# Performance work log

Measured on AMD Instinct MI355X. Metric: run time of the kernel, lower is better.

Reference implementation:

```python
import math
import jax, jax.numpy as jnp
import numpy as np

N_HEADS = 16
HIDDEN = 1024
FACTOR = 256
N_DK = HIDDEN // N_HEADS
B, S = 4, 2048


def _linear_params(key, fan_in, fan_out):
    kw, kb = jax.random.split(key)
    bound = 1.0 / math.sqrt(fan_in)
    W = jax.random.uniform(kw, (fan_in, fan_out), jnp.float32, -bound, bound)
    b = jax.random.uniform(kb, (fan_out,), jnp.float32, -bound, bound)
    return W, b


def setup_inputs() -> dict:
    key = jax.random.key(0)
    ks = jax.random.split(key, 12)
    inp = {
        "query": jax.random.normal(ks[0], (B, S, HIDDEN), jnp.float32),
        "key": jax.random.normal(ks[1], (B, S, HIDDEN), jnp.float32),
        "value": jax.random.normal(ks[2], (B, S, HIDDEN), jnp.float32),
        "mask": jax.random.randint(ks[3], (B, S), 0, 2, jnp.int32),
    }
    names = [("pq", HIDDEN, FACTOR), ("tq", FACTOR, HIDDEN),
             ("pk", HIDDEN, FACTOR), ("tk", FACTOR, HIDDEN),
             ("pv", HIDDEN, FACTOR), ("tv", FACTOR, HIDDEN),
             ("po", HIDDEN, FACTOR), ("to", FACTOR, HIDDEN)]
    for i, (nm, fi, fo) in enumerate(names):
        W, b = _linear_params(ks[4 + i], fi, fo)
        inp[f"W{nm}"], inp[f"b{nm}"] = W, b
    return inp


def _factored(x, Wp, bp, Wt, bt):
    # proj -> leaky_relu(0.2) -> tran
    h = jax.nn.leaky_relu(x @ Wp + bp, negative_slope=0.2)
    return h @ Wt + bt


def reference(query, key, value, mask,
              Wpq, bpq, Wtq, btq, Wpk, bpk, Wtk, btk,
              Wpv, bpv, Wtv, btv, Wpo, bpo, Wto, bto):
    bsize = query.shape[0]

    def split_heads(x):  # [B,S,H*Dk] -> [B,H,S,Dk]
        return x.reshape(bsize, -1, N_HEADS, N_DK).transpose(0, 2, 1, 3)

    q = split_heads(_factored(query, Wpq, bpq, Wtq, btq))
    k = split_heads(_factored(key, Wpk, bpk, Wtk, btk))
    v = split_heads(_factored(value, Wpv, bpv, Wtv, btv))

    scores = jnp.einsum("bhqd,bhkd->bhqk", q, k) / math.sqrt(N_DK)
    m = (mask == 0)[:, None, None, :]  # [B,1,1,S]
    scores = jnp.where(m, jnp.float32(-1e20), scores)
    attn = jax.nn.softmax(scores, axis=-1)
    cv = jnp.einsum("bhqk,bhkd->bhqd", attn, v)
    cv = cv.transpose(0, 2, 1, 3).reshape(bsize, -1, N_HEADS * N_DK)
    # dropout omitted (eval mode / deterministic reference)
    return _factored(cv, Wpo, bpo, Wto, bto)
```

## Files before the change

### kernel.cpp

```cpp
#include <hip/hip_runtime.h>
#include <cstdint>
#include <cstddef>

typedef __bf16 bf16_t;
typedef __bf16 bf16x8 __attribute__((ext_vector_type(8)));
typedef float  f32x4  __attribute__((ext_vector_type(4)));
typedef unsigned int uint32x4 __attribute__((ext_vector_type(4)));
typedef unsigned int uint32x2 __attribute__((ext_vector_type(2)));

#define DEV_INLINE __device__ __forceinline__

constexpr int Bsz = 4, Ssz = 2048, HID = 1024, FAC = 256, NH = 16, DKc = 64;
constexpr int Mrows = Bsz * Ssz;
constexpr float QSCALE = 0.18033688011112042f;

struct Ptr8 { const float* p[8]; };
struct Ptr3 { const float* p[3]; };

DEV_INLINE float fast_exp2(float x) {
#if __has_builtin(__builtin_amdgcn_exp2f)
  return __builtin_amdgcn_exp2f(x);
#else
  return exp2f(x);
#endif
}

DEV_INLINE void async16(const void* g, void* l) {
  __builtin_amdgcn_global_load_lds((const __attribute__((address_space(1))) void*)g,
                                   (__attribute__((address_space(3))) void*)l, 16, 0, 0);
}

DEV_INLINE int SW(int r) { return (r & 3) | ((r >> 1) & 4); }

__global__ __launch_bounds__(256) void k_prep(Ptr8 w, Ptr8 bsrc, const int* __restrict__ mask,
                                              bf16_t* wpt, bf16_t* wtt,
                                              float* bp, float* bt, float* mf, bf16_t* mb) {
  const int z = blockIdx.z;
  if (z == 8) {
    const int bid = blockIdx.y * 32 + blockIdx.x;
    if (bid >= 64) return;
    const int i = bid * 256 + threadIdx.x;
    if (i < 4 * FAC) bp[i] = bsrc.p[i >> 8][i & 255];
    if (i < 4 * HID) bt[i] = bsrc.p[4 + (i >> 10)][i & 1023];
    if (i < Bsz * Ssz) {
      const float m = (mask[i] != 0) ? 1.f : 0.f;
      mf[i] = m;
      mb[i] = (bf16_t)m;
    }
    return;
  }
  const int K = (z < 4) ? HID : FAC;
  const int N = (z < 4) ? FAC : HID;
  if ((int)(blockIdx.x * 32) >= N || (int)(blockIdx.y * 32) >= K) return;
  __shared__ float t[32][33];
  const float* src = w.p[z];
  bf16_t* dst = (z < 4) ? (wpt + (size_t)z * FAC * HID) : (wtt + (size_t)(z - 4) * FAC * HID);
  const int tx = threadIdx.x & 31, ty = threadIdx.x >> 5;
  const int kb = blockIdx.y * 32, nb = blockIdx.x * 32;
#pragma unroll
  for (int j = 0; j < 4; ++j)
    t[ty + j * 8][tx] = src[(size_t)(kb + ty + j * 8) * N + nb + tx];
  __syncthreads();
#pragma unroll
  for (int j = 0; j < 4; ++j)
    dst[(size_t)(nb + ty + j * 8) * K + kb + tx] = (bf16_t)t[tx][ty + j * 8];
}

template <int CAST_A, typename OUT_T>
__global__ __launch_bounds__(256) void k_gemmP(Ptr3 Asrc,
                                               const bf16_t* __restrict__ Aall,
                                               const bf16_t* __restrict__ Bt_,
                                               const float* __restrict__ biasAll,
                                               OUT_T* __restrict__ Call,
                                               int K,
                                               long long Az, long long Bz, long long Cz, int biasz) {
  constexpr int LDTA = CAST_A ? 40 : 32;
  __shared__ __align__(16) bf16_t As[2][64 * LDTA];
  __shared__ __align__(16) bf16_t Bs[2][128 * 32];

  const int z = blockIdx.z;
  const bf16_t* Bt = Bt_ + (size_t)z * Bz;
  const float* bias = biasAll + (size_t)z * biasz;
  OUT_T* C = Call + (size_t)z * Cz;

  const int tid = threadIdx.x;
  const int lane = tid & 63, wave = tid >> 6;
  const int quad = lane >> 4, l16 = lane & 15;
  const int m0 = blockIdx.y * 64, n0 = blockIdx.x * 128;

  const int arow = wave * 16 + (lane >> 2), akc = (lane & 3) * 8;
  const bf16_t* gB0 = Bt + (size_t)(n0 + arow) * K + akc;
  const bf16_t* gB1 = gB0 + (size_t)64 * K;

  const float* gAf = nullptr;
  const bf16_t* gA = nullptr;
  const int crow = tid >> 2, chalf = (tid & 3) * 8;
  if (CAST_A) gAf = Asrc.p[z] + (size_t)(m0 + crow) * K + chalf;
  else        gA  = Aall + (size_t)z * Az + (size_t)(m0 + arow) * K + akc;

  async16(gB0, Bs[0] + wave * 512);
  async16(gB1, Bs[0] + 2048 + wave * 512);
  if (CAST_A) {
    f32x4 x0 = *(const f32x4*)gAf;
    f32x4 x1 = *(const f32x4*)(gAf + 4);
    union { bf16_t h[8]; uint32x4 u; } o;
#pragma unroll
    for (int j = 0; j < 4; ++j) { o.h[j] = (bf16_t)x0[j]; o.h[4 + j] = (bf16_t)x1[j]; }
    *(uint32x4*)(As[0] + crow * LDTA + chalf) = o.u;
  } else {
    async16(gA, As[0] + wave * 512);
  }

  f32x4 acc[4][2] = {};
  const int nk = K / 32;

  for (int it = 0; it < nk; ++it) {
    const int cur = it & 1, nxt = cur ^ 1;
    __syncthreads();

    f32x4 xa, xb;
    const int k1 = (it + 1) * 32;
    if (it + 1 < nk) {
      async16(gB0 + k1, Bs[nxt] + wave * 512);
      async16(gB1 + k1, Bs[nxt] + 2048 + wave * 512);
      if (CAST_A) {
        xa = *(const f32x4*)(gAf + k1);
        xb = *(const f32x4*)(gAf + k1 + 4);
      } else {
        async16(gA + k1, As[nxt] + wave * 512);
      }
    }

    bf16x8 af[4], bfr[2];
#pragma unroll
    for (int i = 0; i < 4; ++i)
      af[i] = *(const bf16x8*)(As[cur] + (i * 16 + l16) * LDTA + quad * 8);
#pragma unroll
    for (int i = 0; i < 2; ++i)
      bfr[i] = *(const bf16x8*)(Bs[cur] + (wave * 32 + i * 16 + l16) * 32 + quad * 8);
#pragma unroll
    for (int mi = 0; mi < 4; ++mi)
#pragma unroll
      for (int ni = 0; ni < 2; ++ni)
        acc[mi][ni] = __builtin_amdgcn_mfma_f32_16x16x32_bf16(af[mi], bfr[ni], acc[mi][ni], 0, 0, 0);

    if (CAST_A && it + 1 < nk) {
      union { bf16_t h[8]; uint32x4 u; } o;
#pragma unroll
      for (int j = 0; j < 4; ++j) { o.h[j] = (bf16_t)xa[j]; o.h[4 + j] = (bf16_t)xb[j]; }
      *(uint32x4*)(As[nxt] + crow * LDTA + chalf) = o.u;
    }
  }

#pragma unroll
  for (int mi = 0; mi < 4; ++mi) {
    const int rbase = m0 + mi * 16 + quad * 4;
#pragma unroll
    for (int ni = 0; ni < 2; ++ni) {
      const int col = n0 + wave * 32 + ni * 16 + l16;
      const float bv = bias[col];
#pragma unroll
      for (int r = 0; r < 4; ++r) {
        float y = acc[mi][ni][r] + bv;
        y = (y > 0.f) ? y : 0.2f * y;
        C[(size_t)(rbase + r) * FAC + col] = (OUT_T)y;
      }
    }
  }
}

template <int TVW, typename OUT_T>
__global__ __launch_bounds__(256) void k_gemm(const bf16_t* __restrict__ Aall,
                                              const bf16_t* __restrict__ Btall,
                                              const float* __restrict__ biasAll,
                                              OUT_T* __restrict__ Call,
                                              bf16_t* __restrict__ C2,
                                              const float* __restrict__ rowmul,
                                              int N, int K,
                                              long long Az, long long Bz, long long Cz, int biasz,
                                              float sc0, float sc1) {
  __shared__ __align__(16) bf16_t As[2][128 * 32];
  __shared__ __align__(16) bf16_t Bs[2][128 * 32];

  const int z = blockIdx.z;
  const bf16_t* Bt = Btall + (size_t)z * Bz;
  const float* bias = biasAll + (size_t)z * biasz;
  OUT_T* C = Call + (size_t)z * Cz;
  const float scale = (z == 0) ? sc0 : sc1;

  const int tid = threadIdx.x;
  const int lane = tid & 63, wave = tid >> 6;
  const int quad = lane >> 4, l16 = lane & 15;
  const int wr = wave >> 1, wc = wave & 1;
  const int m0 = blockIdx.y * 128, n0 = blockIdx.x * 128;

  const int arow = wave * 16 + (lane >> 2), akc = (lane & 3) * 8;
  const bf16_t* gB0 = Bt + (size_t)(n0 + arow) * K + akc;
  const bf16_t* gB1 = gB0 + (size_t)64 * K;
  const bf16_t* A = Aall + (size_t)z * Az;
  const bf16_t* gA0 = A + (size_t)(m0 + arow) * K + akc;
  const bf16_t* gA1 = gA0 + (size_t)64 * K;

  async16(gB0, Bs[0] + wave * 512);
  async16(gB1, Bs[0] + 2048 + wave * 512);
  async16(gA0, As[0] + wave * 512);
  async16(gA1, As[0] + 2048 + wave * 512);

  f32x4 acc[4][4] = {};
  const int nk = K / 32;

  for (int it = 0; it < nk; ++it) {
    const int cur = it & 1, nxt = cur ^ 1;
    __syncthreads();

    if (it + 1 < nk) {
      const int k1 = (it + 1) * 32;
      async16(gB0 + k1, Bs[nxt] + wave * 512);
      async16(gB1 + k1, Bs[nxt] + 2048 + wave * 512);
      async16(gA0 + k1, As[nxt] + wave * 512);
      async16(gA1 + k1, As[nxt] + 2048 + wave * 512);
    }

    bf16x8 af[4], bfr[4];
#pragma unroll
    for (int i = 0; i < 4; ++i)
      af[i] = *(const bf16x8*)(As[cur] + (wr * 64 + i * 16 + l16) * 32 + quad * 8);
#pragma unroll
    for (int i = 0; i < 4; ++i)
      bfr[i] = *(const bf16x8*)(Bs[cur] + (wc * 64 + i * 16 + l16) * 32 + quad * 8);
#pragma unroll
    for (int mi = 0; mi < 4; ++mi)
#pragma unroll
      for (int ni = 0; ni < 4; ++ni)
        acc[mi][ni] = __builtin_amdgcn_mfma_f32_16x16x32_bf16(af[mi], bfr[ni], acc[mi][ni], 0, 0, 0);
  }

  if (TVW && z == 2) {
#pragma unroll
    for (int mi = 0; mi < 4; ++mi) {
      const int rbase = m0 + wr * 64 + mi * 16 + quad * 4;
      const int bb = rbase >> 11, s = rbase & 2047;
      float rmv[4];
#pragma unroll
      for (int r = 0; r < 4; ++r) rmv[r] = rowmul[rbase + r];
#pragma unroll
      for (int ni = 0; ni < 4; ++ni) {
        const int col = n0 + wc * 64 + ni * 16 + l16;
        const float bv = bias[col];
        const int h = col >> 6, d = col & 63;
        union { bf16_t e[4]; uint32x2 u; } p;
#pragma unroll
        for (int r = 0; r < 4; ++r) p.e[r] = (bf16_t)((acc[mi][ni][r] + bv) * rmv[r]);
        *(uint32x2*)(C2 + (((size_t)((bb * NH + h) * DKc + d)) << 11) + s) = p.u;
      }
    }
    return;
  }

#pragma unroll
  for (int mi = 0; mi < 4; ++mi) {
    const int rbase = m0 + wr * 64 + mi * 16 + quad * 4;
#pragma unroll
    for (int ni = 0; ni < 4; ++ni) {
      const int col = n0 + wc * 64 + ni * 16 + l16;
      const float bv = bias[col];
#pragma unroll
      for (int r = 0; r < 4; ++r) {
        float y = (acc[mi][ni][r] + bv) * scale;
        C[(size_t)(rbase + r) * N + col] = (OUT_T)y;
      }
    }
  }
}

__global__ __launch_bounds__(512, 4) void k_attn(const bf16_t* __restrict__ qkv,
                                                 const bf16_t* __restrict__ mb,
                                                 bf16_t* __restrict__ cv) {
  __shared__ __align__(16) bf16_t Ks[2][64 * 64];
  __shared__ __align__(16) bf16_t Vt[2][64 * 64];
  __shared__ __align__(16) bf16_t Ml[Ssz];

  const int qt = blockIdx.x, h = blockIdx.y, b = blockIdx.z;
  const bf16_t* qp = qkv;
  const bf16_t* kp = qkv + (size_t)Mrows * HID;
  const bf16_t* vtp = qkv + 2 * (size_t)Mrows * HID + (size_t)(b * NH + h) * DKc * Ssz;

  const int tid = threadIdx.x;
  const int lane = tid & 63, wave = tid >> 6;
  const int quad = lane >> 4, l16 = lane & 15;

  const int r0 = wave * 8 + (lane >> 3);
  const int c0 = ((lane & 7) ^ SW(r0)) * 8;
  const int ldsOff = wave * 512;
  const bf16_t* kgA = kp + (size_t)(b * Ssz + r0) * HID + h * DKc + c0;
  const bf16_t* vgA = vtp + (size_t)r0 * Ssz + c0;

  *(uint32x2*)(Ml + tid * 4) = *(const uint32x2*)(mb + (size_t)b * Ssz + tid * 4);
  async16(kgA, Ks[0] + ldsOff);
  async16(vgA, Vt[0] + ldsOff);

  bf16x8 aq0[2], aq1[2];
#pragma unroll
  for (int g = 0; g < 2; ++g) {
    const size_t qrow = (size_t)(b * Ssz + qt * 256 + g * 128 + wave * 16 + l16) * HID + h * DKc + quad * 8;
    aq0[g] = *(const bf16x8*)(qp + qrow);
    aq1[g] = *(const bf16x8*)(qp + qrow + 32);
  }
  __syncthreads();

  const int krow = 8 * (l16 >> 2) + (l16 & 3);
  f32x4 acc[2][4] = {};
  f32x4 dacc[2] = {};
  const bf16x8 zfrag = {};

  for (int kt = 0; kt < 32; ++kt) {
    const int cur = kt & 1, nxt = cur ^ 1;
    if (kt < 31) {
      const size_t ko = (size_t)(kt + 1) * 64 * HID;
      const int vo = (kt + 1) * 64;
      async16(kgA + ko, Ks[nxt] + ldsOff);
      async16(vgA + vo, Vt[nxt] + ldsOff);
    }

    union U { uint32x4 u; bf16x8 h; } ap0[2], ap1[2];
    constexpr int koff[4] = {0, 4, 32, 36};
#pragma unroll
    for (int ks = 0; ks < 4; ++ks) {
      const int row = krow + koff[ks];
      const int sw = SW(row);
      bf16x8 a0 = *(const bf16x8*)(Ks[cur] + row * 64 + (quad ^ sw) * 8);
      bf16x8 a1 = *(const bf16x8*)(Ks[cur] + row * 64 + ((quad + 4) ^ sw) * 8);
#pragma unroll
      for (int g = 0; g < 2; ++g) {
        f32x4 c = {};
        c = __builtin_amdgcn_mfma_f32_16x16x32_bf16(a0, aq0[g], c, 0, 0, 0);
        c = __builtin_amdgcn_mfma_f32_16x16x32_bf16(a1, aq1[g], c, 0, 0, 0);
        union { bf16_t h[2]; uint32_t u; } p01, p23;
        p01.h[0] = (bf16_t)fast_exp2(c[0]);
        p01.h[1] = (bf16_t)fast_exp2(c[1]);
        p23.h[0] = (bf16_t)fast_exp2(c[2]);
        p23.h[1] = (bf16_t)fast_exp2(c[3]);
        U& t = (ks < 2) ? ap0[g] : ap1[g];
        t.u[(ks & 1) * 2] = p01.u;
        t.u[(ks & 1) * 2 + 1] = p23.u;
      }
    }

    bf16x8 mr0 = *(const bf16x8*)(Ml + kt * 64 + quad * 8);
    bf16x8 mr1 = *(const bf16x8*)(Ml + kt * 64 + 32 + quad * 8);
    if (l16 != 0) { mr0 = zfrag; mr1 = zfrag; }
#pragma unroll
    for (int g = 0; g < 2; ++g) {
      dacc[g] = __builtin_amdgcn_mfma_f32_16x16x32_bf16(ap0[g].h, mr0, dacc[g], 0, 0, 0);
      dacc[g] = __builtin_amdgcn_mfma_f32_16x16x32_bf16(ap1[g].h, mr1, dacc[g], 0, 0, 0);
    }

#pragma unroll
    for (int d = 0; d < 4; ++d) {
      const int row = d * 16 + l16;
      const int sw = SW(row);
      bf16x8 bv0 = *(const bf16x8*)(Vt[cur] + row * 64 + (quad ^ sw) * 8);
      bf16x8 bv1 = *(const bf16x8*)(Vt[cur] + row * 64 + ((quad + 4) ^ sw) * 8);
#pragma unroll
      for (int g = 0; g < 2; ++g) {
        acc[g][d] = __builtin_amdgcn_mfma_f32_16x16x32_bf16(ap0[g].h, bv0, acc[g][d], 0, 0, 0);
        acc[g][d] = __builtin_amdgcn_mfma_f32_16x16x32_bf16(ap1[g].h, bv1, acc[g][d], 0, 0, 0);
      }
    }

    __syncthreads();
  }

#pragma unroll
  for (int g = 0; g < 2; ++g) {
    const size_t obase = (size_t)(b * Ssz + qt * 256 + g * 128 + wave * 16 + quad * 4) * HID + h * DKc + l16;
#pragma unroll
    for (int r = 0; r < 4; ++r) {
      const float denom = __shfl(dacc[g][r], lane & 48, 64);
      const float rl = 1.f / denom;
#pragma unroll
      for (int d = 0; d < 4; ++d)
        cv[obase + (size_t)r * HID + d * 16] = (bf16_t)(acc[g][d][r] * rl);
    }
  }
}

extern "C" void kernel_launch(void* const* d_in, const int* in_sizes, int n_in,
                              void* d_out, int out_size, void* d_ws, size_t ws_size,
                              hipStream_t stream) {
  (void)in_sizes; (void)n_in; (void)out_size; (void)ws_size;
  const float* q_in = (const float*)d_in[0];
  const float* k_in = (const float*)d_in[1];
  const float* v_in = (const float*)d_in[2];
  const int* mask = (const int*)d_in[3];

  bf16_t* XB = (bf16_t*)d_ws;
  bf16_t* H3 = XB + (size_t)3 * Mrows * HID;
  bf16_t* CV = H3 + (size_t)3 * Mrows * FAC;
  bf16_t* WPT = CV + (size_t)Mrows * HID;
  bf16_t* WTT = WPT + (size_t)4 * FAC * HID;
  float* BP = (float*)(WTT + (size_t)4 * FAC * HID);
  float* BT = BP + 4 * FAC;
  float* MF = BT + 4 * HID;
  bf16_t* MB = (bf16_t*)(MF + Mrows);
  bf16_t* VTg = XB + 2 * (size_t)Mrows * HID;

  Ptr8 w;
  w.p[0] = (const float*)d_in[4];  w.p[1] = (const float*)d_in[8];
  w.p[2] = (const float*)d_in[12]; w.p[3] = (const float*)d_in[16];
  w.p[4] = (const float*)d_in[6];  w.p[5] = (const float*)d_in[10];
  w.p[6] = (const float*)d_in[14]; w.p[7] = (const float*)d_in[18];
  Ptr8 bs;
  bs.p[0] = (const float*)d_in[5];  bs.p[1] = (const float*)d_in[9];
  bs.p[2] = (const float*)d_in[13]; bs.p[3] = (const float*)d_in[17];
  bs.p[4] = (const float*)d_in[7];  bs.p[5] = (const float*)d_in[11];
  bs.p[6] = (const float*)d_in[15]; bs.p[7] = (const float*)d_in[19];
  hipLaunchKernelGGL(k_prep, dim3(32, 32, 9), dim3(256), 0, stream, w, bs, mask,
                     WPT, WTT, BP, BT, MF, MB);

  Ptr3 xs; xs.p[0] = q_in; xs.p[1] = k_in; xs.p[2] = v_in;
  Ptr3 nullp; nullp.p[0] = nullp.p[1] = nullp.p[2] = nullptr;

  hipLaunchKernelGGL((k_gemmP<1, bf16_t>), dim3(2, Mrows / 64, 3), dim3(256), 0, stream,
                     xs, (const bf16_t*)nullptr, WPT, BP, H3,
                     HID, 0LL, (long long)FAC * HID, (long long)Mrows * FAC, FAC);

  hipLaunchKernelGGL((k_gemm<1, bf16_t>), dim3(HID / 128, Mrows / 128, 3), dim3(256), 0, stream,
                     H3, WTT, BT, XB, VTg, MF,
                     HID, FAC, (long long)Mrows * FAC, (long long)FAC * HID, (long long)Mrows * HID, HID,
                     QSCALE, 1.f);

  hipLaunchKernelGGL(k_attn, dim3(Ssz / 256, NH, Bsz), dim3(512), 0, stream, XB, MB, CV);

  hipLaunchKernelGGL((k_gemmP<0, bf16_t>), dim3(2, Mrows / 64, 1), dim3(256), 0, stream,
                     nullp, CV, WPT + (size_t)3 * FAC * HID, BP + 3 * FAC, H3,
                     HID, 0LL, 0LL, 0LL, 0);

  hipLaunchKernelGGL((k_gemm<0, float>), dim3(HID / 128, Mrows / 128, 1), dim3(256), 0, stream,
                     H3, WTT + (size_t)3 * FAC * HID, BT + 3 * HID, (float*)d_out, (bf16_t*)nullptr,
                     (const float*)nullptr, HID, FAC, 0LL, 0LL, 0LL, 0, 1.f, 1.f);
}
```

Measured before the change: 340.6 us.

## Deepen async load pipelines to multi-buffer with vmcnt-based barriers across GEMMs and attention

Replaces double-buffered global-to-LDS loads with 3–4 stage ring buffers that prefetch two tiles ahead, and swaps __syncthreads for explicit s_waitcnt vmcnt(N) plus s_barrier so that waves stall only on the tile they are about to consume. It applies this to the projection GEMM, the transform GEMMs and the attention kernel. The bf16-input output projection now uses the 128x128 tiled GEMM with a leaky-relu epilogue. LDS use grows, which may lower occupancy, and the hand-written vmcnt counts must match the number of outstanding loads exactly.

```diff
diff --git a/kernel.cpp b/kernel.cpp
--- a/kernel.cpp
+++ b/kernel.cpp
@@ -29,6 +29,11 @@
   __builtin_amdgcn_global_load_lds((const __attribute__((address_space(1))) void*)g,
                                    (__attribute__((address_space(3))) void*)l, 16, 0, 0);
 }
+
+#define WBAR(N) do { \
+  asm volatile("s_waitcnt vmcnt(" #N ") lgkmcnt(0)" ::: "memory"); \
+  __builtin_amdgcn_s_barrier(); \
+} while (0)
 
 DEV_INLINE int SW(int r) { return (r & 3) | ((r >> 1) & 4); }
 
@@ -66,91 +71,89 @@
     dst[(size_t)(nb + ty + j * 8) * K + kb + tx] = (bf16_t)t[tx][ty + j * 8];
 }
 
-template <int CAST_A, typename OUT_T>
-__global__ __launch_bounds__(256) void k_gemmP(Ptr3 Asrc,
-                                               const bf16_t* __restrict__ Aall,
-                                               const bf16_t* __restrict__ Bt_,
-                                               const float* __restrict__ biasAll,
-                                               OUT_T* __restrict__ Call,
-                                               int K,
-                                               long long Az, long long Bz, long long Cz, int biasz) {
-  constexpr int LDTA = CAST_A ? 40 : 32;
-  __shared__ __align__(16) bf16_t As[2][64 * LDTA];
-  __shared__ __align__(16) bf16_t Bs[2][128 * 32];
+__global__ __launch_bounds__(256, 2) void k_gemmP2(Ptr3 Asrc,
+                                                   const bf16_t* __restrict__ Bt_,
+                                                   const float* __restrict__ biasAll,
+                                                   bf16_t* __restrict__ Call) {
+  __shared__ __align__(16) bf16_t As[3][64 * 40];
+  __shared__ __align__(16) bf16_t Bs[4][128 * 32];
 
   const int z = blockIdx.z;
-  const bf16_t* Bt = Bt_ + (size_t)z * Bz;
-  const float* bias = biasAll + (size_t)z * biasz;
-  OUT_T* C = Call + (size_t)z * Cz;
+  const bf16_t* Bt = Bt_ + (size_t)z * FAC * HID;
+  const float* bias = biasAll + z * FAC;
+  bf16_t* C = Call + (size_t)z * Mrows * FAC;
 
   const int tid = threadIdx.x;
   const int lane = tid & 63, wave = tid >> 6;
   const int quad = lane >> 4, l16 = lane & 15;
   const int m0 = blockIdx.y * 64, n0 = blockIdx.x * 128;
 
-  const int arow = wave * 16 + (lane >> 2), akc = (lane & 3) * 8;
-  const bf16_t* gB0 = Bt + (size_t)(n0 + arow) * K + akc;
-  const bf16_t* gB1 = gB0 + (size_t)64 * K;
-
-  const float* gAf = nullptr;
-  const bf16_t* gA = nullptr;
+  const int brow = wave * 16 + (lane >> 2), bkc = (lane & 3) * 8;
+  const bf16_t* gB0 = Bt + (size_t)(n0 + brow) * HID + bkc;
+  const bf16_t* gB1 = gB0 + (size_t)64 * HID;
+
   const int crow = tid >> 2, chalf = (tid & 3) * 8;
-  if (CAST_A) gAf = Asrc.p[z] + (size_t)(m0 + crow) * K + chalf;
-  else        gA  = Aall + (size_t)z * Az + (size_t)(m0 + arow) * K + akc;
-
-  async16(gB0, Bs[0] + wave * 512);
-  async16(gB1, Bs[0] + 2048 + wave * 512);
-  if (CAST_A) {
-    f32x4 x0 = *(const f32x4*)gAf;
-    f32x4 x1 = *(const f32x4*)(gAf + 4);
+  const float* gAf = Asrc.p[z] + (size_t)(m0 + crow) * HID + chalf;
+
+#define ASYNCB(t, buf)                                \
+  do {                                                \
+    const int k0_ = (t) * 32;                         \
+    async16(gB0 + k0_, Bs[buf] + wave * 512);         \
+    async16(gB1 + k0_, Bs[buf] + 2048 + wave * 512);  \
+  } while (0)
+
+  {
+    f32x4 pa = *(const f32x4*)gAf;
+    f32x4 pb = *(const f32x4*)(gAf + 4);
+    __builtin_amdgcn_sched_barrier(0);
+    ASYNCB(0, 0);
+    ASYNCB(1, 1);
     union { bf16_t h[8]; uint32x4 u; } o;
 #pragma unroll
-    for (int j = 0; j < 4; ++j) { o.h[j] = (bf16_t)x0[j]; o.h[4 + j] = (bf16_t)x1[j]; }
-    *(uint32x4*)(As[0] + crow * LDTA + chalf) = o.u;
-  } else {
-    async16(gA, As[0] + wave * 512);
+    for (int j = 0; j < 4; ++j) { o.h[j] = (bf16_t)pa[j]; o.h[4 + j] = (bf16_t)pb[j]; }
+    *(uint32x4*)(As[0] + crow * 40 + chalf) = o.u;
   }
 
   f32x4 acc[4][2] = {};
-  const int nk = K / 32;
+  constexpr int nk = 32;
 
   for (int it = 0; it < nk; ++it) {
-    const int cur = it & 1, nxt = cur ^ 1;
-    __syncthreads();
-
     f32x4 xa, xb;
     const int k1 = (it + 1) * 32;
     if (it + 1 < nk) {
-      async16(gB0 + k1, Bs[nxt] + wave * 512);
-      async16(gB1 + k1, Bs[nxt] + 2048 + wave * 512);
-      if (CAST_A) {
-        xa = *(const f32x4*)(gAf + k1);
-        xb = *(const f32x4*)(gAf + k1 + 4);
-      } else {
-        async16(gA + k1, As[nxt] + wave * 512);
-      }
-    }
-
+      xa = *(const f32x4*)(gAf + k1);
+      xb = *(const f32x4*)(gAf + k1 + 4);
+    }
+    __builtin_amdgcn_sched_barrier(0);
+    if (it + 2 < nk) ASYNCB(it + 2, (it + 2) & 3);
+
+    if (it + 2 < nk)      WBAR(6);
+    else if (it + 1 < nk) WBAR(4);
+    else                  WBAR(0);
+
+    const bf16_t* Ac = As[it % 3];
+    const bf16_t* Bc = Bs[it & 3];
     bf16x8 af[4], bfr[2];
 #pragma unroll
     for (int i = 0; i < 4; ++i)
-      af[i] = *(const bf16x8*)(As[cur] + (i * 16 + l16) * LDTA + quad * 8);
+      af[i] = *(const bf16x8*)(Ac + (i * 16 + l16) * 40 + quad * 8);
 #pragma unroll
     for (int i = 0; i < 2; ++i)
-      bfr[i] = *(const bf16x8*)(Bs[cur] + (wave * 32 + i * 16 + l16) * 32 + quad * 8);
+      bfr[i] = *(const bf16x8*)(Bc + (wave * 32 + i * 16 + l16) * 32 + quad * 8);
 #pragma unroll
     for (int mi = 0; mi < 4; ++mi)
 #pragma unroll
       for (int ni = 0; ni < 2; ++ni)
         acc[mi][ni] = __builtin_amdgcn_mfma_f32_16x16x32_bf16(af[mi], bfr[ni], acc[mi][ni], 0, 0, 0);
 
-    if (CAST_A && it + 1 < nk) {
+    if (it + 1 < nk) {
       union { bf16_t h[8]; uint32x4 u; } o;
 #pragma unroll
       for (int j = 0; j < 4; ++j) { o.h[j] = (bf16_t)xa[j]; o.h[4 + j] = (bf16_t)xb[j]; }
-      *(uint32x4*)(As[nxt] + crow * LDTA + chalf) = o.u;
-    }
-  }
+      *(uint32x4*)(As[(it + 1) % 3] + crow * 40 + chalf) = o.u;
+    }
+  }
+#undef ASYNCB
 
 #pragma unroll
   for (int mi = 0; mi < 4; ++mi) {
@@ -163,30 +166,28 @@
       for (int r = 0; r < 4; ++r) {
         float y = acc[mi][ni][r] + bv;
         y = (y > 0.f) ? y : 0.2f * y;
-        C[(size_t)(rbase + r) * FAC + col] = (OUT_T)y;
+        C[(size_t)(rbase + r) * FAC + col] = (bf16_t)y;
       }
     }
   }
 }
 
-template <int TVW, typename OUT_T>
-__global__ __launch_bounds__(256) void k_gemm(const bf16_t* __restrict__ Aall,
-                                              const bf16_t* __restrict__ Btall,
-                                              const float* __restrict__ biasAll,
-                                              OUT_T* __restrict__ Call,
-                                              bf16_t* __restrict__ C2,
-                                              const float* __restrict__ rowmul,
-                                              int N, int K,
-                                              long long Az, long long Bz, long long Cz, int biasz,
-                                              float sc0, float sc1) {
-  __shared__ __align__(16) bf16_t As[2][128 * 32];
-  __shared__ __align__(16) bf16_t Bs[2][128 * 32];
+template <int EPI, typename OUT_T>
+__global__ __launch_bounds__(256, 2) void k_gemmQ(const bf16_t* __restrict__ Aall,
+                                                  const bf16_t* __restrict__ Btall,
+                                                  const float* __restrict__ biasAll,
+                                                  OUT_T* __restrict__ Call,
+                                                  bf16_t* __restrict__ C2,
+                                                  const float* __restrict__ rowmul,
+                                                  int N, int K,
+                                                  long long Az, long long Bz, long long Cz, int biasz) {
+  __shared__ __align__(16) bf16_t As[4][128 * 32];
+  __shared__ __align__(16) bf16_t Bs[4][128 * 32];
 
   const int z = blockIdx.z;
   const bf16_t* Bt = Btall + (size_t)z * Bz;
   const float* bias = biasAll + (size_t)z * biasz;
   OUT_T* C = Call + (size_t)z * Cz;
-  const float scale = (z == 0) ? sc0 : sc1;
 
   const int tid = threadIdx.x;
   const int lane = tid & 63, wave = tid >> 6;
@@ -201,41 +202,46 @@
   const bf16_t* gA0 = A + (size_t)(m0 + arow) * K + akc;
   const bf16_t* gA1 = gA0 + (size_t)64 * K;
 
-  async16(gB0, Bs[0] + wave * 512);
-  async16(gB1, Bs[0] + 2048 + wave * 512);
-  async16(gA0, As[0] + wave * 512);
-  async16(gA1, As[0] + 2048 + wave * 512);
+#define STAGEQ(t, buf)                               \
+  do {                                               \
+    const int k0_ = (t) * 32;                        \
+    async16(gA0 + k0_, As[buf] + wave * 512);        \
+    async16(gA1 + k0_, As[buf] + 2048 + wave * 512); \
+    async16(gB0 + k0_, Bs[buf] + wave * 512);        \
+    async16(gB1 + k0_, Bs[buf] + 2048 + wave * 512); \
+  } while (0)
+
+  const int nk = K / 32;
+  STAGEQ(0, 0);
+  STAGEQ(1, 1);
 
   f32x4 acc[4][4] = {};
-  const int nk = K / 32;
 
   for (int it = 0; it < nk; ++it) {
-    const int cur = it & 1, nxt = cur ^ 1;
-    __syncthreads();
-
-    if (it + 1 < nk) {
-      const int k1 = (it + 1) * 32;
-      async16(gB0 + k1, Bs[nxt] + wave * 512);
-      async16(gB1 + k1, Bs[nxt] + 2048 + wave * 512);
-      async16(gA0 + k1, As[nxt] + wave * 512);
-      async16(gA1 + k1, As[nxt] + 2048 + wave * 512);
-    }
-
+    if (it + 2 < nk) STAGEQ(it + 2, (it + 2) & 3);
+
+    if (it + 2 < nk)      WBAR(8);
+    else if (it + 1 < nk) WBAR(4);
+    else                  WBAR(0);
+
+    const bf16_t* Ac = As[it & 3];
+    const bf16_t* Bc = Bs[it & 3];
     bf16x8 af[4], bfr[4];
 #pragma unroll
     for (int i = 0; i < 4; ++i)
-      af[i] = *(const bf16x8*)(As[cur] + (wr * 64 + i * 16 + l16) * 32 + quad * 8);
+      af[i] = *(const bf16x8*)(Ac + (wr * 64 + i * 16 + l16) * 32 + quad * 8);
 #pragma unroll
     for (int i = 0; i < 4; ++i)
-      bfr[i] = *(const bf16x8*)(Bs[cur] + (wc * 64 + i * 16 + l16) * 32 + quad * 8);
+      bfr[i] = *(const bf16x8*)(Bc + (wc * 64 + i * 16 + l16) * 32 + quad * 8);
 #pragma unroll
     for (int mi = 0; mi < 4; ++mi)
 #pragma unroll
       for (int ni = 0; ni < 4; ++ni)
         acc[mi][ni] = __builtin_amdgcn_mfma_f32_16x16x32_bf16(af[mi], bfr[ni], acc[mi][ni], 0, 0, 0);
   }
-
-  if (TVW && z == 2) {
+#undef STAGEQ
+
+  if (EPI == 1 && z == 2) {
 #pragma unroll
     for (int mi = 0; mi < 4; ++mi) {
       const int rbase = m0 + wr * 64 + mi * 16 + quad * 4;
@@ -247,16 +253,17 @@
       for (int ni = 0; ni < 4; ++ni) {
         const int col = n0 + wc * 64 + ni * 16 + l16;
         const float bv = bias[col];
-        const int h = col >> 6, d = col & 63;
+        const int hh = col >> 6, d = col & 63;
         union { bf16_t e[4]; uint32x2 u; } p;
 #pragma unroll
         for (int r = 0; r < 4; ++r) p.e[r] = (bf16_t)((acc[mi][ni][r] + bv) * rmv[r]);
-        *(uint32x2*)(C2 + (((size_t)((bb * NH + h) * DKc + d)) << 11) + s) = p.u;
+        *(uint32x2*)(C2 + (((size_t)((bb * NH + hh) * DKc + d)) << 11) + s) = p.u;
       }
     }
     return;
   }
 
+  const float scale = (EPI == 1 && z == 0) ? QSCALE : 1.f;
 #pragma unroll
   for (int mi = 0; mi < 4; ++mi) {
     const int rbase = m0 + wr * 64 + mi * 16 + quad * 4;
@@ -267,6 +274,7 @@
 #pragma unroll
       for (int r = 0; r < 4; ++r) {
         float y = (acc[mi][ni][r] + bv) * scale;
+        if (EPI == 0) y = (y > 0.f) ? y : 0.2f * y;
         C[(size_t)(rbase + r) * N + col] = (OUT_T)y;
       }
     }
@@ -276,8 +284,8 @@
 __global__ __launch_bounds__(512, 4) void k_attn(const bf16_t* __restrict__ qkv,
                                                  const bf16_t* __restrict__ mb,
                                                  bf16_t* __restrict__ cv) {
-  __shared__ __align__(16) bf16_t Ks[2][64 * 64];
-  __shared__ __align__(16) bf16_t Vt[2][64 * 64];
+  __shared__ __align__(16) bf16_t Ks[4][64 * 64];
+  __shared__ __align__(16) bf16_t Vt[4][64 * 64];
   __shared__ __align__(16) bf16_t Ml[Ssz];
 
   const int qt = blockIdx.x, h = blockIdx.y, b = blockIdx.z;
@@ -295,9 +303,15 @@
   const bf16_t* kgA = kp + (size_t)(b * Ssz + r0) * HID + h * DKc + c0;
   const bf16_t* vgA = vtp + (size_t)r0 * Ssz + c0;
 
+#define STAGEA(t, buf)                                          \
+  do {                                                          \
+    async16(kgA + (size_t)(t) * 64 * HID, Ks[buf] + ldsOff);    \
+    async16(vgA + (t) * 64, Vt[buf] + ldsOff);                  \
+  } while (0)
+
   *(uint32x2*)(Ml + tid * 4) = *(const uint32x2*)(mb + (size_t)b * Ssz + tid * 4);
-  async16(kgA, Ks[0] + ldsOff);
-  async16(vgA, Vt[0] + ldsOff);
+  STAGEA(0, 0);
+  STAGEA(1, 1);
 
   bf16x8 aq0[2], aq1[2];
 #pragma unroll
@@ -306,7 +320,6 @@
     aq0[g] = *(const bf16x8*)(qp + qrow);
     aq1[g] = *(const bf16x8*)(qp + qrow + 32);
   }
-  __syncthreads();
 
   const int krow = 8 * (l16 >> 2) + (l16 & 3);
   f32x4 acc[2][4] = {};
@@ -314,13 +327,14 @@
   const bf16x8 zfrag = {};
 
   for (int kt = 0; kt < 32; ++kt) {
-    const int cur = kt & 1, nxt = cur ^ 1;
-    if (kt < 31) {
-      const size_t ko = (size_t)(kt + 1) * 64 * HID;
-      const int vo = (kt + 1) * 64;
-      async16(kgA + ko, Ks[nxt] + ldsOff);
-      async16(vgA + vo, Vt[nxt] + ldsOff);
-    }
+    if (kt + 2 < 32) STAGEA(kt + 2, (kt + 2) & 3);
+
+    if (kt + 2 < 32)      WBAR(4);
+    else if (kt + 1 < 32) WBAR(2);
+    else                  WBAR(0);
+
+    const bf16_t* Kc = Ks[kt & 3];
+    const bf16_t* Vc = Vt[kt & 3];
 
     union U { uint32x4 u; bf16x8 h; } ap0[2], ap1[2];
     constexpr int koff[4] = {0, 4, 32, 36};
@@ -328,8 +342,8 @@
     for (int ks = 0; ks < 4; ++ks) {
       const int row = krow + koff[ks];
       const int sw = SW(row);
-      bf16x8 a0 = *(const bf16x8*)(Ks[cur] + row * 64 + (quad ^ sw) * 8);
-      bf16x8 a1 = *(const bf16x8*)(Ks[cur] + row * 64 + ((quad + 4) ^ sw) * 8);
+      bf16x8 a0 = *(const bf16x8*)(Kc + row * 64 + (quad ^ sw) * 8);
+      bf16x8 a1 = *(const bf16x8*)(Kc + row * 64 + ((quad + 4) ^ sw) * 8);
 #pragma unroll
       for (int g = 0; g < 2; ++g) {
         f32x4 c = {};
@@ -359,17 +373,16 @@
     for (int d = 0; d < 4; ++d) {
       const int row = d * 16 + l16;
       const int sw = SW(row);
-      bf16x8 bv0 = *(const bf16x8*)(Vt[cur] + row * 64 + (quad ^ sw) * 8);
-      bf16x8 bv1 = *(const bf16x8*)(Vt[cur] + row * 64 + ((quad + 4) ^ sw) * 8);
+      bf16x8 bv0 = *(const bf16x8*)(Vc + row * 64 + (quad ^ sw) * 8);
+      bf16x8 bv1 = *(const bf16x8*)(Vc + row * 64 + ((quad + 4) ^ sw) * 8);
 #pragma unroll
       for (int g = 0; g < 2; ++g) {
         acc[g][d] = __builtin_amdgcn_mfma_f32_16x16x32_bf16(ap0[g].h, bv0, acc[g][d], 0, 0, 0);
         acc[g][d] = __builtin_amdgcn_mfma_f32_16x16x32_bf16(ap1[g].h, bv1, acc[g][d], 0, 0, 0);
       }
     }
-
-    __syncthreads();
-  }
+  }
+#undef STAGEA
 
 #pragma unroll
   for (int g = 0; g < 2; ++g) {
@@ -419,24 +432,21 @@
                      WPT, WTT, BP, BT, MF, MB);
 
   Ptr3 xs; xs.p[0] = q_in; xs.p[1] = k_in; xs.p[2] = v_in;
-  Ptr3 nullp; nullp.p[0] = nullp.p[1] = nullp.p[2] = nullptr;
-
-  hipLaunchKernelGGL((k_gemmP<1, bf16_t>), dim3(2, Mrows / 64, 3), dim3(256), 0, stream,
-                     xs, (const bf16_t*)nullptr, WPT, BP, H3,
-                     HID, 0LL, (long long)FAC * HID, (long long)Mrows * FAC, FAC);
-
-  hipLaunchKernelGGL((k_gemm<1, bf16_t>), dim3(HID / 128, Mrows / 128, 3), dim3(256), 0, stream,
+
+  hipLaunchKernelGGL(k_gemmP2, dim3(2, Mrows / 64, 3), dim3(256), 0, stream,
+                     xs, WPT, BP, H3);
+
+  hipLaunchKernelGGL((k_gemmQ<1, bf16_t>), dim3(HID / 128, Mrows / 128, 3), dim3(256), 0, stream,
                      H3, WTT, BT, XB, VTg, MF,
-                     HID, FAC, (long long)Mrows * FAC, (long long)FAC * HID, (long long)Mrows * HID, HID,
-                     QSCALE, 1.f);
+                     HID, FAC, (long long)Mrows * FAC, (long long)FAC * HID, (long long)Mrows * HID, HID);
 
   hipLaunchKernelGGL(k_attn, dim3(Ssz / 256, NH, Bsz), dim3(512), 0, stream, XB, MB, CV);
 
-  hipLaunchKernelGGL((k_gemmP<0, bf16_t>), dim3(2, Mrows / 64, 1), dim3(256), 0, stream,
-                     nullp, CV, WPT + (size_t)3 * FAC * HID, BP + 3 * FAC, H3,
-                     HID, 0LL, 0LL, 0LL, 0);
-
-  hipLaunchKernelGGL((k_gemm<0, float>), dim3(HID / 128, Mrows / 128, 1), dim3(256), 0, stream,
+  hipLaunchKernelGGL((k_gemmQ<0, bf16_t>), dim3(FAC / 128, Mrows / 128, 1), dim3(256), 0, stream,
+                     CV, WPT + (size_t)3 * FAC * HID, BP + 3 * FAC, H3, (bf16_t*)nullptr,
+                     (const float*)nullptr, FAC, HID, 0LL, 0LL, 0LL, 0);
+
+  hipLaunchKernelGGL((k_gemmQ<2, float>), dim3(HID / 128, Mrows / 128, 1), dim3(256), 0, stream,
                      H3, WTT + (size_t)3 * FAC * HID, BT + 3 * HID, (float*)d_out, (bf16_t*)nullptr,
-                     (const float*)nullptr, HID, FAC, 0LL, 0LL, 0LL, 0, 1.f, 1.f);
-}
+                     (const float*)nullptr, HID, FAC, 0LL, 0LL, 0LL, 0);
+}
```

Result: no change. 335.3 us (-1.6%).
